# Performance work log

Measured on AMD Instinct MI355X. Metric: run time of the kernel, lower is better.

## Reference

```python
import jax, jax.numpy as jnp
import numpy as np

B, S, IN, OUT = 8, 4096, 1024, 1024


def setup_inputs() -> dict:
    key = jax.random.key(0)
    k1, k2, k3, k4, k5 = jax.random.split(key, 5)
    x = jax.random.normal(k1, (B, S, IN), dtype=jnp.float32)
    # pre-quantized int8 weight buffer [out, in]
    weight = jax.random.randint(k2, (OUT, IN), -127, 128, dtype=jnp.int32).astype(jnp.int8)
    bias = jax.random.normal(k3, (OUT,), dtype=jnp.float32) * 0.1
    # per-channel weight clip values (>0)
    w_clip_val = jax.random.uniform(k4, (OUT,), minval=0.5, maxval=2.0, dtype=jnp.float32)
    # smoothquant per-input-channel activation scaling factors (>0)
    smoothquant_scale = jax.random.uniform(k5, (IN,), minval=0.5, maxval=2.0, dtype=jnp.float32)
    return {"x": x, "weight": weight, "bias": bias,
            "w_clip_val": w_clip_val, "smoothquant_scale": smoothquant_scale}


def reference(x, weight, bias, w_clip_val, smoothquant_scale):
    # i8i8_aiu semantics for weight_quant_type='per_channel',
    # activ_quant_type='per_token' (symmetric -> zero_shift == 0), smoothquant=True.
    # 1) smoothquant: scale activations prior to quantization
    xs = x / smoothquant_scale                                   # [B,S,IN]
    # 2) per-token symmetric int8 quantization of activations
    a_scale = jnp.max(jnp.abs(xs), axis=-1, keepdims=True) / 127.0  # [B,S,1]
    a_scale = jnp.maximum(a_scale, 1e-8)
    x_int = jnp.round(jnp.clip(xs / a_scale, -127.0, 127.0)).astype(jnp.int8)
    acc = jax.lax.dot_general(x_int, weight,
                              dimension_numbers=(((2,), (1,)), ((), ())),
                              preferred_element_type=jnp.int32)
    # 4) fused dequant (per-token act scale * per-channel weight scale) + bias
    w_scale = w_clip_val / 127.0                                 # [OUT]
    return acc.astype(jnp.float32) * a_scale * w_scale + bias
```

## Files before the change

### kernel.cpp

```cpp
#include <hip/hip_runtime.h>
#include <stdint.h>

#define T_TOK 32768
#define NIN   1024
#define NOUT  1024
#define BM    32
#define NTHR  512

typedef int v4i  __attribute__((ext_vector_type(4)));
typedef int v16i __attribute__((ext_vector_type(16)));

__global__ __launch_bounds__(256) void repack_w_frag(const int* __restrict__ w,
                                                     uint32_t* __restrict__ wf) {
  const int gid  = blockIdx.x * 256 + threadIdx.x;
  const int lane = gid & 63;
  const int ks   = (gid >> 6) & 31;
  const int nt   = gid >> 11;
  const int n    = nt * 32 + (lane & 31);
  const int kb   = ks * 32 + (lane >> 5) * 16;
  const int* src = w + (size_t)n * NIN + kb;
  uint32_t d[4];
#pragma unroll
  for (int q = 0; q < 4; ++q) {
    const int4 v = ((const int4*)src)[q];
    d[q] = (uint32_t)(v.x & 0xff) | ((uint32_t)(v.y & 0xff) << 8) |
           ((uint32_t)(v.z & 0xff) << 16) | ((uint32_t)(v.w & 0xff) << 24);
  }
  ((uint4*)wf)[gid] = make_uint4(d[0], d[1], d[2], d[3]);
}

__global__ __launch_bounds__(NTHR) void fused_w8a8(
    const float* __restrict__ x,
    const uint8_t* __restrict__ wf,
    const float* __restrict__ sq,
    const float* __restrict__ wclip,
    const float* __restrict__ bias,
    float* __restrict__ out)
{
  __shared__ __align__(16) uint8_t A8[BM * NIN];
  __shared__ float ascale_s[BM];

  const int tid  = threadIdx.x;
  const int lane = tid & 63;
  const int w    = tid >> 6;
  const int t0   = blockIdx.x * BM;

  const float4* sq4 = (const float4*)sq;
  float4 rs[4];
#pragma unroll
  for (int j = 0; j < 4; ++j) {
    const float4 s = sq4[j * 64 + lane];
    rs[j].x = __builtin_amdgcn_rcpf(s.x);
    rs[j].y = __builtin_amdgcn_rcpf(s.y);
    rs[j].z = __builtin_amdgcn_rcpf(s.z);
    rs[j].w = __builtin_amdgcn_rcpf(s.w);
  }
#pragma unroll
  for (int i = 0; i < 4; ++i) {
    const int tl = w * 4 + i;
    const float4* xr = (const float4*)(x + (size_t)(t0 + tl) * NIN);
    float4 v[4];
    float m = 0.f;
#pragma unroll
    for (int j = 0; j < 4; ++j) {
      float4 a = xr[j * 64 + lane];
      a.x *= rs[j].x; a.y *= rs[j].y; a.z *= rs[j].z; a.w *= rs[j].w;
      v[j] = a;
      m = fmaxf(m, fmaxf(fmaxf(fabsf(a.x), fabsf(a.y)),
                         fmaxf(fabsf(a.z), fabsf(a.w))));
    }
#pragma unroll
    for (int off = 1; off < 64; off <<= 1) m = fmaxf(m, __shfl_xor(m, off));
    const float as = fmaxf(m * (1.f / 127.f), 1e-8f);
    if (lane == 0) ascale_s[tl] = as;
    const float ia = __builtin_amdgcn_rcpf(as);
#pragma unroll
    for (int j = 0; j < 4; ++j) {
      const int q0 = (int)rintf(fminf(fmaxf(v[j].x * ia, -127.f), 127.f));
      const int q1 = (int)rintf(fminf(fmaxf(v[j].y * ia, -127.f), 127.f));
      const int q2 = (int)rintf(fminf(fmaxf(v[j].z * ia, -127.f), 127.f));
      const int q3 = (int)rintf(fminf(fmaxf(v[j].w * ia, -127.f), 127.f));
      const uint32_t d = (uint32_t)(q0 & 0xff) | ((uint32_t)(q1 & 0xff) << 8) |
                         ((uint32_t)(q2 & 0xff) << 16) | ((uint32_t)(q3 & 0xff) << 24);
      const int di = j * 64 + lane;
      const int ch = (di >> 2) ^ (tl & 7);
      *(uint32_t*)(A8 + tl * NIN + ch * 16 + (di & 3) * 4) = d;
    }
  }
  __syncthreads();

  v16i acc[4] = {};

  auto ldB = [&](int ks, int nt) -> v4i {
    return *(const v4i*)(wf +
        ((((size_t)(w * 4 + nt) * 32 + ks) * 64 + lane) << 4));
  };
  auto ldA = [&](int ks) -> v4i {
    const int row = lane & 31;
    const int ch  = (ks * 2 + (lane >> 5)) ^ (row & 7);
    return *(const v4i*)(A8 + row * NIN + ch * 16);
  };

  v4i B[4][4];
#pragma unroll
  for (int p = 0; p < 4; ++p)
#pragma unroll
    for (int nt = 0; nt < 4; ++nt) B[p][nt] = ldB(p, nt);

  for (int ks = 0; ks < 32; ks += 4) {
#pragma unroll
    for (int p = 0; p < 4; ++p) {
      const v4i af = ldA(ks + p);
#pragma unroll
      for (int nt = 0; nt < 4; ++nt)
        acc[nt] = __builtin_amdgcn_mfma_i32_32x32x32_i8(af, B[p][nt], acc[nt], 0, 0, 0);
      if (ks + 4 + p < 32) {
#pragma unroll
        for (int nt = 0; nt < 4; ++nt) B[p][nt] = ldB(ks + 4 + p, nt);
      }
    }
  }

#pragma unroll
  for (int nt = 0; nt < 4; ++nt) {
    const int n = (w * 4 + nt) * 32 + (lane & 31);
    const float wsc = wclip[n] * (1.f / 127.f);
    const float bs  = bias[n];
#pragma unroll
    for (int reg = 0; reg < 16; ++reg) {
      const int r = (reg & 3) + 8 * (reg >> 2) + 4 * (lane >> 5);
      out[(size_t)(t0 + r) * NOUT + n] =
          (float)acc[nt][reg] * ascale_s[r] * wsc + bs;
    }
  }
}

extern "C" void kernel_launch(void* const* d_in, const int* in_sizes, int n_in,
                              void* d_out, int out_size, void* d_ws, size_t ws_size,
                              hipStream_t stream) {
  const float* x      = (const float*)d_in[0];
  const int*   weight = (const int*)d_in[1];
  const float* bias   = (const float*)d_in[2];
  const float* wclip  = (const float*)d_in[3];
  const float* sq     = (const float*)d_in[4];
  float* out = (float*)d_out;

  uint32_t* wfrag = (uint32_t*)d_ws;

  repack_w_frag<<<(NOUT * NIN / 16) / 256, 256, 0, stream>>>(weight, wfrag);
  fused_w8a8<<<T_TOK / BM, NTHR, 0, stream>>>(x, (const uint8_t*)wfrag,
                                              sq, wclip, bias, out);
}
```

Baseline: 92.10 us.

## Split quantization into separate kernel and retile GEMM to 128x256 with LDS staging

Moves per-token activation quantization into its own kernel, which writes int8 activations in MFMA fragment layout to workspace. The GEMM becomes a separate kernel with 128-token by 256-output tiles. It stages A into LDS through direct global-to-LDS loads, uses XCD-aware block mapping, raises priority around the MFMA sequence, and writes output with nontemporal stores. The aim is more reuse of B per block and better MFMA utilization than the fused 32-row tile, which reloaded the full weight for every 32 tokens. The cost is an extra round trip of int8 activations (32 MB write and read) through global memory and one more launch.

After: 93.37 us. Within noise of the previous version (+1.4%).

```diff
diff --git a/kernel.cpp b/kernel.cpp
--- a/kernel.cpp
+++ b/kernel.cpp
@@ -4,11 +4,19 @@
 #define T_TOK 32768
 #define NIN   1024
 #define NOUT  1024
-#define BM    32
-#define NTHR  512
-
-typedef int v4i  __attribute__((ext_vector_type(4)));
-typedef int v16i __attribute__((ext_vector_type(16)));
+
+typedef int   v4i  __attribute__((ext_vector_type(4)));
+typedef int   v16i __attribute__((ext_vector_type(16)));
+typedef float v4f  __attribute__((ext_vector_type(4)));
+
+#define MFMA_I8(a, b, c) __builtin_amdgcn_mfma_i32_32x32x32_i8(a, b, c, 0, 0, 0)
+
+__device__ __forceinline__ void gload_lds16(const void* g, void* l) {
+  __builtin_amdgcn_global_load_lds(
+      (const __attribute__((address_space(1))) unsigned int*)g,
+      (__attribute__((address_space(3))) unsigned int*)l, 16, 0, 0);
+}
+
 
 __global__ __launch_bounds__(256) void repack_w_frag(const int* __restrict__ w,
                                                      uint32_t* __restrict__ wf) {
@@ -29,108 +37,171 @@
   ((uint4*)wf)[gid] = make_uint4(d[0], d[1], d[2], d[3]);
 }
 
-__global__ __launch_bounds__(NTHR) void fused_w8a8(
-    const float* __restrict__ x,
+__global__ __launch_bounds__(512) void quant2(const float* __restrict__ x,
+                                              const float* __restrict__ sq,
+                                              uint32_t* __restrict__ afw,
+                                              float* __restrict__ asc) {
+  __shared__ __align__(16) uint8_t Af[32 * NIN];
+
+  const int tid  = threadIdx.x;
+  const int lane = tid & 63;
+  const int w    = tid >> 6;
+  const int t0   = blockIdx.x * 32;
+
+  {
+    const v4f* sq4 = (const v4f*)sq;
+    v4f rs[4];
+#pragma unroll
+    for (int j = 0; j < 4; ++j) {
+      const v4f s = sq4[j * 64 + lane];
+      rs[j].x = __builtin_amdgcn_rcpf(s.x);
+      rs[j].y = __builtin_amdgcn_rcpf(s.y);
+      rs[j].z = __builtin_amdgcn_rcpf(s.z);
+      rs[j].w = __builtin_amdgcn_rcpf(s.w);
+    }
+#pragma unroll
+    for (int i = 0; i < 4; ++i) {
+      const int tl = w * 4 + i;
+      const v4f* xr = (const v4f*)(x + (size_t)(t0 + tl) * NIN);
+      v4f v[4];
+      float m = 0.f;
+#pragma unroll
+      for (int j = 0; j < 4; ++j) {
+        v4f a = __builtin_nontemporal_load(&xr[j * 64 + lane]);
+        a.x *= rs[j].x; a.y *= rs[j].y; a.z *= rs[j].z; a.w *= rs[j].w;
+        v[j] = a;
+        m = fmaxf(m, fmaxf(fmaxf(fabsf(a.x), fabsf(a.y)),
+                           fmaxf(fabsf(a.z), fabsf(a.w))));
+      }
+#pragma unroll
+      for (int off = 1; off < 64; off <<= 1) m = fmaxf(m, __shfl_xor(m, off));
+      const float as = fmaxf(m * (1.f / 127.f), 1e-8f);
+      if (lane == 0) asc[t0 + tl] = as;
+      const float ia = __builtin_amdgcn_rcpf(as);
+#pragma unroll
+      for (int j = 0; j < 4; ++j) {
+        const int q0 = (int)rintf(fminf(fmaxf(v[j].x * ia, -127.f), 127.f));
+        const int q1 = (int)rintf(fminf(fmaxf(v[j].y * ia, -127.f), 127.f));
+        const int q2 = (int)rintf(fminf(fmaxf(v[j].z * ia, -127.f), 127.f));
+        const int q3 = (int)rintf(fminf(fmaxf(v[j].w * ia, -127.f), 127.f));
+        const uint32_t d = (uint32_t)(q0 & 0xff) | ((uint32_t)(q1 & 0xff) << 8) |
+                           ((uint32_t)(q2 & 0xff) << 16) | ((uint32_t)(q3 & 0xff) << 24);
+        const int di   = j * 64 + lane;
+        const int ksw  = di >> 3;
+        const int h    = (di >> 2) & 1;
+        const int slot = ((tl ^ (ksw & 7)) & 31) + 32 * h;
+        *(uint32_t*)(&Af[(ksw * 64 + slot) * 16 + (di & 3) * 4]) = d;
+      }
+    }
+  }
+  __syncthreads();
+
+  v4i* dst = (v4i*)afw + (size_t)blockIdx.x * 2048;
+#pragma unroll
+  for (int p = 0; p < 4; ++p) {
+    const int cg = p * 512 + tid;
+    const int ks = cg >> 6;
+    const int lc = (cg & ~31) | ((cg ^ (ks & 7)) & 31);
+    __builtin_nontemporal_store(*(const v4i*)(&Af[lc * 16]), &dst[cg]);
+  }
+}
+
+__global__ __launch_bounds__(256, 2) void gemm2(
+    const uint8_t* __restrict__ af,
     const uint8_t* __restrict__ wf,
-    const float* __restrict__ sq,
+    const float* __restrict__ asc,
     const float* __restrict__ wclip,
     const float* __restrict__ bias,
     float* __restrict__ out)
 {
-  __shared__ __align__(16) uint8_t A8[BM * NIN];
-  __shared__ float ascale_s[BM];
+  __shared__ __align__(16) uint8_t As[64 * 1024];
+
+  const int g   = blockIdx.x;
+  const int xcd = g & 7;
+  const int j   = g >> 3;
+  const int T   = xcd * 32 + (j >> 2);
+  const int nb  = j & 3;
 
   const int tid  = threadIdx.x;
   const int lane = tid & 63;
   const int w    = tid >> 6;
-  const int t0   = blockIdx.x * BM;
-
-  const float4* sq4 = (const float4*)sq;
-  float4 rs[4];
-#pragma unroll
-  for (int j = 0; j < 4; ++j) {
-    const float4 s = sq4[j * 64 + lane];
-    rs[j].x = __builtin_amdgcn_rcpf(s.x);
-    rs[j].y = __builtin_amdgcn_rcpf(s.y);
-    rs[j].z = __builtin_amdgcn_rcpf(s.z);
-    rs[j].w = __builtin_amdgcn_rcpf(s.w);
-  }
-#pragma unroll
-  for (int i = 0; i < 4; ++i) {
-    const int tl = w * 4 + i;
-    const float4* xr = (const float4*)(x + (size_t)(t0 + tl) * NIN);
-    float4 v[4];
-    float m = 0.f;
-#pragma unroll
-    for (int j = 0; j < 4; ++j) {
-      float4 a = xr[j * 64 + lane];
-      a.x *= rs[j].x; a.y *= rs[j].y; a.z *= rs[j].z; a.w *= rs[j].w;
-      v[j] = a;
-      m = fmaxf(m, fmaxf(fmaxf(fabsf(a.x), fabsf(a.y)),
-                         fmaxf(fabsf(a.z), fabsf(a.w))));
-    }
-#pragma unroll
-    for (int off = 1; off < 64; off <<= 1) m = fmaxf(m, __shfl_xor(m, off));
-    const float as = fmaxf(m * (1.f / 127.f), 1e-8f);
-    if (lane == 0) ascale_s[tl] = as;
-    const float ia = __builtin_amdgcn_rcpf(as);
-#pragma unroll
-    for (int j = 0; j < 4; ++j) {
-      const int q0 = (int)rintf(fminf(fmaxf(v[j].x * ia, -127.f), 127.f));
-      const int q1 = (int)rintf(fminf(fmaxf(v[j].y * ia, -127.f), 127.f));
-      const int q2 = (int)rintf(fminf(fmaxf(v[j].z * ia, -127.f), 127.f));
-      const int q3 = (int)rintf(fminf(fmaxf(v[j].w * ia, -127.f), 127.f));
-      const uint32_t d = (uint32_t)(q0 & 0xff) | ((uint32_t)(q1 & 0xff) << 8) |
-                         ((uint32_t)(q2 & 0xff) << 16) | ((uint32_t)(q3 & 0xff) << 24);
-      const int di = j * 64 + lane;
-      const int ch = (di >> 2) ^ (tl & 7);
-      *(uint32_t*)(A8 + tl * NIN + ch * 16 + (di & 3) * 4) = d;
-    }
-  }
+
+  const uint8_t* Abase = af + ((size_t)(T * 4) << 15);
+  const uint8_t* Bb    = wf + ((size_t)(nb * 8 + w * 2) << 15) + lane * 16;
+
+  auto stage_half = [&](int h) {
+#pragma unroll
+    for (int p = 0; p < 16; ++p) {
+      const int off = p * 4096 + tid * 16;
+      const int mt  = off >> 14;
+      const int inr = off & 16383;
+      gload_lds16(Abase + mt * 32768 + h * 16384 + inr, As + off);
+    }
+  };
+  auto ldA = [&](int mt, int ksl) -> v4i {
+    return *(const v4i*)(As + (((mt * 16 + ksl) * 64) + lane) * 16);
+  };
+  auto ldB = [&](int ks, int ntl) -> v4i {
+    return *(const v4i*)(Bb + ntl * 32768 + ks * 1024);
+  };
+
+  v16i acc[4][2] = {};
+  v4i Bae[2], Bao[2];
+
+  stage_half(0);
+  Bae[0] = ldB(0, 0); Bae[1] = ldB(0, 1);
+  Bao[0] = ldB(1, 0); Bao[1] = ldB(1, 1);
   __syncthreads();
 
-  v16i acc[4] = {};
-
-  auto ldB = [&](int ks, int nt) -> v4i {
-    return *(const v4i*)(wf +
-        ((((size_t)(w * 4 + nt) * 32 + ks) * 64 + lane) << 4));
-  };
-  auto ldA = [&](int ks) -> v4i {
-    const int row = lane & 31;
-    const int ch  = (ks * 2 + (lane >> 5)) ^ (row & 7);
-    return *(const v4i*)(A8 + row * NIN + ch * 16);
-  };
-
-  v4i B[4][4];
-#pragma unroll
-  for (int p = 0; p < 4; ++p)
-#pragma unroll
-    for (int nt = 0; nt < 4; ++nt) B[p][nt] = ldB(p, nt);
-
-  for (int ks = 0; ks < 32; ks += 4) {
-#pragma unroll
-    for (int p = 0; p < 4; ++p) {
-      const v4i af = ldA(ks + p);
-#pragma unroll
-      for (int nt = 0; nt < 4; ++nt)
-        acc[nt] = __builtin_amdgcn_mfma_i32_32x32x32_i8(af, B[p][nt], acc[nt], 0, 0, 0);
-      if (ks + 4 + p < 32) {
-#pragma unroll
-        for (int nt = 0; nt < 4; ++nt) B[p][nt] = ldB(ks + 4 + p, nt);
+#define STEP(KSL, BREG, KN)                                                  \
+  do {                                                                       \
+    v4i a[4];                                                                \
+    _Pragma("unroll") for (int mt = 0; mt < 4; ++mt) a[mt] = ldA(mt, (KSL)); \
+    __builtin_amdgcn_s_setprio(1);                                           \
+    _Pragma("unroll") for (int mt = 0; mt < 4; ++mt) {                       \
+      acc[mt][0] = MFMA_I8(a[mt], BREG[0], acc[mt][0]);                      \
+      acc[mt][1] = MFMA_I8(a[mt], BREG[1], acc[mt][1]);                      \
+    }                                                                        \
+    __builtin_amdgcn_s_setprio(0);                                           \
+    if ((KN) < 32) { BREG[0] = ldB((KN), 0); BREG[1] = ldB((KN), 1); }       \
+  } while (0)
+
+#pragma unroll
+  for (int h = 0; h < 2; ++h) {
+    if (h == 1) {
+      __syncthreads();
+      stage_half(1);
+      __syncthreads();
+    }
+#pragma unroll
+    for (int kp = 0; kp < 16; kp += 2) {
+      const int ks = h * 16 + kp;
+      STEP(kp,     Bae, ks + 2);
+      STEP(kp + 1, Bao, ks + 3);
+    }
+  }
+#undef STEP
+
+  const int hr = 4 * (lane >> 5);
+#pragma unroll
+  for (int mt = 0; mt < 4; ++mt) {
+    const int t0 = T * 128 + mt * 32;
+    float ascv[16];
+#pragma unroll
+    for (int reg = 0; reg < 16; ++reg)
+      ascv[reg] = asc[t0 + (reg & 3) + 8 * (reg >> 2) + hr];
+#pragma unroll
+    for (int ntl = 0; ntl < 2; ++ntl) {
+      const int n = nb * 256 + (w * 2 + ntl) * 32 + (lane & 31);
+      const float wsc = wclip[n] * (1.f / 127.f);
+      const float bs  = bias[n];
+#pragma unroll
+      for (int reg = 0; reg < 16; ++reg) {
+        const int r = t0 + (reg & 3) + 8 * (reg >> 2) + hr;
+        __builtin_nontemporal_store(
+            (float)acc[mt][ntl][reg] * ascv[reg] * wsc + bs,
+            &out[(size_t)r * NOUT + n]);
       }
-    }
-  }
-
-#pragma unroll
-  for (int nt = 0; nt < 4; ++nt) {
-    const int n = (w * 4 + nt) * 32 + (lane & 31);
-    const float wsc = wclip[n] * (1.f / 127.f);
-    const float bs  = bias[n];
-#pragma unroll
-    for (int reg = 0; reg < 16; ++reg) {
-      const int r = (reg & 3) + 8 * (reg >> 2) + 4 * (lane >> 5);
-      out[(size_t)(t0 + r) * NOUT + n] =
-          (float)acc[nt][reg] * ascale_s[r] * wsc + bs;
     }
   }
 }
@@ -145,9 +216,13 @@
   const float* sq     = (const float*)d_in[4];
   float* out = (float*)d_out;
 
-  uint32_t* wfrag = (uint32_t*)d_ws;
+  uint8_t* ws = (uint8_t*)d_ws;
+  uint32_t* wfrag = (uint32_t*)ws;
+  uint32_t* afrag = (uint32_t*)(ws + (1u << 20));
+  float*    ascp  = (float*)(ws + (1u << 20) + ((size_t)T_TOK * NIN));
 
   repack_w_frag<<<(NOUT * NIN / 16) / 256, 256, 0, stream>>>(weight, wfrag);
-  fused_w8a8<<<T_TOK / BM, NTHR, 0, stream>>>(x, (const uint8_t*)wfrag,
-                                              sq, wclip, bias, out);
-}
+  quant2<<<T_TOK / 32, 512, 0, stream>>>(x, sq, afrag, ascp);
+  gemm2<<<1024, 256, 0, stream>>>((const uint8_t*)afrag, (const uint8_t*)wfrag,
+                                  ascp, wclip, bias, out);
+}
```

## Warp-specialize fused kernel into quantize producers and MFMA consumers with double-buffered tiles

Applied to the files above, without the earlier changes.

Each block now handles two 64-token tiles. The first is quantized by all waves. Then four waves quantize the second tile into a second LDS buffer while the other four run the int8 MFMA GEMM on the first, so activation loading overlaps with matrix work. Consumer waves compute 64x128 sub-tiles in two halves of N, reusing each B fragment across two M tiles. The LDS layout is changed to a fragment-chunked swizzle, and the kernel adds nontemporal loads and stores, s_setprio around the MFMAs, and launch bounds of 2 blocks per CU. LDS use grows to 128KB per block, which may limit occupancy, and the GEMM phase now runs on only half the waves.

Measured after the change: 102.2 us. 1.11x slower.

```diff
diff --git a/kernel.cpp b/kernel.cpp
--- a/kernel.cpp
+++ b/kernel.cpp
@@ -4,11 +4,14 @@
 #define T_TOK 32768
 #define NIN   1024
 #define NOUT  1024
-#define BM    32
+#define BM    64
 #define NTHR  512
 
-typedef int v4i  __attribute__((ext_vector_type(4)));
-typedef int v16i __attribute__((ext_vector_type(16)));
+typedef int   v4i  __attribute__((ext_vector_type(4)));
+typedef int   v16i __attribute__((ext_vector_type(16)));
+typedef float v4f  __attribute__((ext_vector_type(4)));
+
+#define MFMA_I8(a, b, c) __builtin_amdgcn_mfma_i32_32x32x32_i8(a, b, c, 0, 0, 0)
 
 __global__ __launch_bounds__(256) void repack_w_frag(const int* __restrict__ w,
                                                      uint32_t* __restrict__ wf) {
@@ -29,7 +32,7 @@
   ((uint4*)wf)[gid] = make_uint4(d[0], d[1], d[2], d[3]);
 }
 
-__global__ __launch_bounds__(NTHR) void fused_w8a8(
+__global__ __launch_bounds__(NTHR, 2) void fused_pc(
     const float* __restrict__ x,
     const uint8_t* __restrict__ wf,
     const float* __restrict__ sq,
@@ -37,43 +40,29 @@
     const float* __restrict__ bias,
     float* __restrict__ out)
 {
-  __shared__ __align__(16) uint8_t A8[BM * NIN];
-  __shared__ float ascale_s[BM];
+  __shared__ __align__(16) uint8_t Af[2][BM * NIN];
+  __shared__ float ascale_s[2][BM];
 
   const int tid  = threadIdx.x;
   const int lane = tid & 63;
   const int w    = tid >> 6;
-  const int t0   = blockIdx.x * BM;
-
-  const float4* sq4 = (const float4*)sq;
-  float4 rs[4];
-#pragma unroll
-  for (int j = 0; j < 4; ++j) {
-    const float4 s = sq4[j * 64 + lane];
-    rs[j].x = __builtin_amdgcn_rcpf(s.x);
-    rs[j].y = __builtin_amdgcn_rcpf(s.y);
-    rs[j].z = __builtin_amdgcn_rcpf(s.z);
-    rs[j].w = __builtin_amdgcn_rcpf(s.w);
-  }
-#pragma unroll
-  for (int i = 0; i < 4; ++i) {
-    const int tl = w * 4 + i;
-    const float4* xr = (const float4*)(x + (size_t)(t0 + tl) * NIN);
-    float4 v[4];
-    float m = 0.f;
+  const int bt0  = blockIdx.x * (2 * BM);
+
+  const v4f* sq4 = (const v4f*)sq;
+
+  auto make_rs = [&](v4f* rs) {
 #pragma unroll
     for (int j = 0; j < 4; ++j) {
-      float4 a = xr[j * 64 + lane];
-      a.x *= rs[j].x; a.y *= rs[j].y; a.z *= rs[j].z; a.w *= rs[j].w;
-      v[j] = a;
-      m = fmaxf(m, fmaxf(fmaxf(fabsf(a.x), fabsf(a.y)),
-                         fmaxf(fabsf(a.z), fabsf(a.w))));
-    }
-#pragma unroll
-    for (int off = 1; off < 64; off <<= 1) m = fmaxf(m, __shfl_xor(m, off));
-    const float as = fmaxf(m * (1.f / 127.f), 1e-8f);
-    if (lane == 0) ascale_s[tl] = as;
-    const float ia = __builtin_amdgcn_rcpf(as);
+      const v4f s = sq4[j * 64 + lane];
+      rs[j].x = __builtin_amdgcn_rcpf(s.x);
+      rs[j].y = __builtin_amdgcn_rcpf(s.y);
+      rs[j].z = __builtin_amdgcn_rcpf(s.z);
+      rs[j].w = __builtin_amdgcn_rcpf(s.w);
+    }
+  };
+
+  auto quant_store = [&](int buf, int tl, const v4f* v, float ia) {
+    const int mt = tl >> 5;
 #pragma unroll
     for (int j = 0; j < 4; ++j) {
       const int q0 = (int)rintf(fminf(fmaxf(v[j].x * ia, -127.f), 127.f));
@@ -82,57 +71,131 @@
       const int q3 = (int)rintf(fminf(fmaxf(v[j].w * ia, -127.f), 127.f));
       const uint32_t d = (uint32_t)(q0 & 0xff) | ((uint32_t)(q1 & 0xff) << 8) |
                          ((uint32_t)(q2 & 0xff) << 16) | ((uint32_t)(q3 & 0xff) << 24);
-      const int di = j * 64 + lane;
-      const int ch = (di >> 2) ^ (tl & 7);
-      *(uint32_t*)(A8 + tl * NIN + ch * 16 + (di & 3) * 4) = d;
-    }
+      const int di   = j * 64 + lane;
+      const int ksw  = di >> 3;
+      const int hh   = (di >> 2) & 1;
+      const int slot = (tl & 31) + 32 * hh;
+      const int chunk = (mt * 32 + ksw) * 64 + (slot ^ (ksw & 7));
+      *(uint32_t*)(&Af[buf][chunk * 16 + (di & 3) * 4]) = d;
+    }
+  };
+
+  auto quant_pair = [&](int buf, int t0, int tl, const v4f* rs) {
+    const v4f* xa = (const v4f*)(x + (size_t)(t0 + tl) * NIN);
+    const v4f* xb = (const v4f*)(x + (size_t)(t0 + tl + 1) * NIN);
+    v4f va[4], vb[4];
+#pragma unroll
+    for (int j = 0; j < 4; ++j) va[j] = __builtin_nontemporal_load(&xa[j * 64 + lane]);
+#pragma unroll
+    for (int j = 0; j < 4; ++j) vb[j] = __builtin_nontemporal_load(&xb[j * 64 + lane]);
+    float ma = 0.f, mb = 0.f;
+#pragma unroll
+    for (int j = 0; j < 4; ++j) {
+      va[j].x *= rs[j].x; va[j].y *= rs[j].y; va[j].z *= rs[j].z; va[j].w *= rs[j].w;
+      vb[j].x *= rs[j].x; vb[j].y *= rs[j].y; vb[j].z *= rs[j].z; vb[j].w *= rs[j].w;
+      ma = fmaxf(ma, fmaxf(fmaxf(fabsf(va[j].x), fabsf(va[j].y)),
+                           fmaxf(fabsf(va[j].z), fabsf(va[j].w))));
+      mb = fmaxf(mb, fmaxf(fmaxf(fabsf(vb[j].x), fabsf(vb[j].y)),
+                           fmaxf(fabsf(vb[j].z), fabsf(vb[j].w))));
+    }
+#pragma unroll
+    for (int off = 1; off < 64; off <<= 1) {
+      ma = fmaxf(ma, __shfl_xor(ma, off));
+      mb = fmaxf(mb, __shfl_xor(mb, off));
+    }
+    const float asa = fmaxf(ma * (1.f / 127.f), 1e-8f);
+    const float asb = fmaxf(mb * (1.f / 127.f), 1e-8f);
+    if (lane == 0) { ascale_s[buf][tl] = asa; ascale_s[buf][tl + 1] = asb; }
+    quant_store(buf, tl,     va, __builtin_amdgcn_rcpf(asa));
+    quant_store(buf, tl + 1, vb, __builtin_amdgcn_rcpf(asb));
+  };
+
+  auto consumer_tile = [&](int buf, int t0g) {
+    const int wc = w - 4;
+#pragma unroll
+    for (int h = 0; h < 2; ++h) {
+      const uint8_t* Bb = wf + ((size_t)(h * 16 + wc * 4) << 15) + (size_t)lane * 16;
+      auto ldB = [&](int ks, int nt) -> v4i {
+        return *(const v4i*)(Bb + nt * 32768 + ks * 1024);
+      };
+      auto ldA = [&](int mt, int ks) -> v4i {
+        return *(const v4i*)(&Af[buf][(((mt * 32 + ks) * 64) + (lane ^ (ks & 7))) << 4]);
+      };
+      v4i Ba[4], Bo[4];
+#pragma unroll
+      for (int nt = 0; nt < 4; ++nt) { Ba[nt] = ldB(0, nt); Bo[nt] = ldB(1, nt); }
+      v16i acc[2][4] = {};
+      for (int ks = 0; ks < 32; ks += 2) {
+        {
+          const v4i a0 = ldA(0, ks), a1 = ldA(1, ks);
+          __builtin_amdgcn_s_setprio(1);
+#pragma unroll
+          for (int nt = 0; nt < 4; ++nt) {
+            acc[0][nt] = MFMA_I8(a0, Ba[nt], acc[0][nt]);
+            acc[1][nt] = MFMA_I8(a1, Ba[nt], acc[1][nt]);
+          }
+          __builtin_amdgcn_s_setprio(0);
+          if (ks + 2 < 32) {
+#pragma unroll
+            for (int nt = 0; nt < 4; ++nt) Ba[nt] = ldB(ks + 2, nt);
+          }
+        }
+        {
+          const v4i a0 = ldA(0, ks + 1), a1 = ldA(1, ks + 1);
+          __builtin_amdgcn_s_setprio(1);
+#pragma unroll
+          for (int nt = 0; nt < 4; ++nt) {
+            acc[0][nt] = MFMA_I8(a0, Bo[nt], acc[0][nt]);
+            acc[1][nt] = MFMA_I8(a1, Bo[nt], acc[1][nt]);
+          }
+          __builtin_amdgcn_s_setprio(0);
+          if (ks + 3 < 32) {
+#pragma unroll
+            for (int nt = 0; nt < 4; ++nt) Bo[nt] = ldB(ks + 3, nt);
+          }
+        }
+      }
+      const int hr = 4 * (lane >> 5);
+#pragma unroll
+      for (int mt = 0; mt < 2; ++mt) {
+        float ascv[16];
+#pragma unroll
+        for (int reg = 0; reg < 16; ++reg)
+          ascv[reg] = ascale_s[buf][mt * 32 + (reg & 3) + 8 * (reg >> 2) + hr];
+#pragma unroll
+        for (int nt = 0; nt < 4; ++nt) {
+          const int n = h * 512 + wc * 128 + nt * 32 + (lane & 31);
+          const float wsc = wclip[n] * (1.f / 127.f);
+          const float bs  = bias[n];
+#pragma unroll
+          for (int reg = 0; reg < 16; ++reg) {
+            const int r = t0g + mt * 32 + (reg & 3) + 8 * (reg >> 2) + hr;
+            __builtin_nontemporal_store(
+                (float)acc[mt][nt][reg] * ascv[reg] * wsc + bs,
+                &out[(size_t)r * NOUT + n]);
+          }
+        }
+      }
+    }
+  };
+
+  {
+    v4f rs[4]; make_rs(rs);
+#pragma unroll
+    for (int p = 0; p < 4; ++p) quant_pair(0, bt0, w * 8 + p * 2, rs);
   }
   __syncthreads();
 
-  v16i acc[4] = {};
-
-  auto ldB = [&](int ks, int nt) -> v4i {
-    return *(const v4i*)(wf +
-        ((((size_t)(w * 4 + nt) * 32 + ks) * 64 + lane) << 4));
-  };
-  auto ldA = [&](int ks) -> v4i {
-    const int row = lane & 31;
-    const int ch  = (ks * 2 + (lane >> 5)) ^ (row & 7);
-    return *(const v4i*)(A8 + row * NIN + ch * 16);
-  };
-
-  v4i B[4][4];
-#pragma unroll
-  for (int p = 0; p < 4; ++p)
-#pragma unroll
-    for (int nt = 0; nt < 4; ++nt) B[p][nt] = ldB(p, nt);
-
-  for (int ks = 0; ks < 32; ks += 4) {
-#pragma unroll
-    for (int p = 0; p < 4; ++p) {
-      const v4i af = ldA(ks + p);
-#pragma unroll
-      for (int nt = 0; nt < 4; ++nt)
-        acc[nt] = __builtin_amdgcn_mfma_i32_32x32x32_i8(af, B[p][nt], acc[nt], 0, 0, 0);
-      if (ks + 4 + p < 32) {
-#pragma unroll
-        for (int nt = 0; nt < 4; ++nt) B[p][nt] = ldB(ks + 4 + p, nt);
-      }
-    }
+  if (w < 4) {
+    v4f rs[4]; make_rs(rs);
+#pragma unroll
+    for (int p = 0; p < 8; ++p) quant_pair(1, bt0 + BM, w * 16 + p * 2, rs);
+  } else {
+    consumer_tile(0, bt0);
   }
-
-#pragma unroll
-  for (int nt = 0; nt < 4; ++nt) {
-    const int n = (w * 4 + nt) * 32 + (lane & 31);
-    const float wsc = wclip[n] * (1.f / 127.f);
-    const float bs  = bias[n];
-#pragma unroll
-    for (int reg = 0; reg < 16; ++reg) {
-      const int r = (reg & 3) + 8 * (reg >> 2) + 4 * (lane >> 5);
-      out[(size_t)(t0 + r) * NOUT + n] =
-          (float)acc[nt][reg] * ascale_s[r] * wsc + bs;
-    }
-  }
+  __syncthreads();
+
+  if (w >= 4) consumer_tile(1, bt0 + BM);
 }
 
 extern "C" void kernel_launch(void* const* d_in, const int* in_sizes, int n_in,
@@ -148,6 +211,6 @@
   uint32_t* wfrag = (uint32_t*)d_ws;
 
   repack_w_frag<<<(NOUT * NIN / 16) / 256, 256, 0, stream>>>(weight, wfrag);
-  fused_w8a8<<<T_TOK / BM, NTHR, 0, stream>>>(x, (const uint8_t*)wfrag,
-                                              sq, wclip, bias, out);
+  fused_pc<<<T_TOK / (2 * BM), NTHR, 0, stream>>>(x, (const uint8_t*)wfrag,
+                                                  sq, wclip, bias, out);
 }
```
